# Performance work log

Measured on AMD Instinct MI355X. Metric: run time of the kernel, lower is better.

## Reference

```python
import jax, jax.numpy as jnp
import numpy as np

N = 8192          # batch_size == number of graph nodes
F1 = 64
F2 = 64
D_IN = F1 * F2    # 4096, = int(sqrt(in_feats))**2
D_OUT = 4096      # out_feats, must equal F1*F2 for the final reshape
ALPHA = 0.2       # LeakyReLU negative slope


def setup_inputs() -> dict:
    key = jax.random.key(0)
    k_x, k_w, k_a = jax.random.split(key, 3)
    x = jax.random.normal(k_x, (N, F1, F2), dtype=jnp.float32)
    # torch Linear weight layout: [out_feats, in_feats]; xavier-uniform-ish scale
    lim_w = float(np.sqrt(6.0 / (D_IN + D_OUT)) * np.sqrt(2.0))
    W = jax.random.uniform(k_w, (D_OUT, D_IN), dtype=jnp.float32, minval=-lim_w, maxval=lim_w)
    lim_a = float(np.sqrt(6.0 / (1 + 2 * D_OUT)))
    a = jax.random.uniform(k_a, (1, 2 * D_OUT), dtype=jnp.float32, minval=-lim_a, maxval=lim_a)
    return {"x": x, "W": W, "a": a}


def reference(x, W, a):
    b, f1, f2 = x.shape
    x_flat = x.reshape(b, f1 * f2)                 # [N, D_in]
    h = x_flat @ W.T                               # [N, D_out]
    # scores[i,j] = leakyrelu(cat(h_i, h_j) @ a.T) = leakyrelu(h_i.a1 + h_j.a2)
    a1 = a[0, :D_OUT]                              # [D_out]
    a2 = a[0, D_OUT:]                              # [D_out]
    s1 = h @ a1                                    # [N]
    s2 = h @ a2                                    # [N]
    e = s1[:, None] + s2[None, :]                  # [N, N]
    e = jnp.where(e > 0, e, ALPHA * e)             # LeakyReLU
    attention = jax.nn.softmax(e, axis=-1)         # [N, N]
    # dropout=0.0 (eval-mode / deterministic reference)
    out = attention @ h                            # [N, D_out]
    return out.reshape(b, f1, f2)
```

## Files before the change

kernel.cpp:

```cpp
#include <hip/hip_runtime.h>
#include <hip/hip_bf16.h>
#include <stdint.h>


typedef float  f32x4  __attribute__((ext_vector_type(4)));
typedef __bf16 bf16x8 __attribute__((ext_vector_type(8)));

#define AS1 __attribute__((address_space(1)))
#define AS3 __attribute__((address_space(3)))

constexpr int NB  = 8192;
constexpr int DF  = 4096;
constexpr int CH  = 64;
constexpr int NCH = NB / CH;

constexpr int GK  = DF;
constexpr int BKK = 64;
constexpr int NT2 = GK / BKK;

__device__ __forceinline__ uint16_t f2bf_u(float f) {
  union { float f; uint32_t u; } x; x.f = f;
  return (uint16_t)((x.u + 0x7FFFu + ((x.u >> 16) & 1u)) >> 16);
}
__device__ __forceinline__ float bfu2f(uint16_t v) {
  union { uint32_t u; float f; } x; x.u = ((uint32_t)v) << 16;
  return x.f;
}

__global__ __launch_bounds__(256) void cvt_f32_to_bf16(
    const float* __restrict__ in, uint16_t* __restrict__ out, int n4) {
  int idx = blockIdx.x * 256 + threadIdx.x;
  int stride = gridDim.x * 256;
  for (int i = idx; i < n4; i += stride) {
    float4 v = ((const float4*)in)[i];
    ushort4 o;
    o.x = f2bf_u(v.x); o.y = f2bf_u(v.y); o.z = f2bf_u(v.z); o.w = f2bf_u(v.w);
    ((ushort4*)out)[i] = o;
  }
}


#define STAGE_A(tt, half) do {                                                 \
  const uint16_t* g0_ = Ag + (size_t)((half) * 128) * GK + (size_t)(tt) * BKK; \
  uint32_t d_ = ((uint32_t)((tt) & 1)) * 32768u + (uint32_t)(half) * 8192u +   \
                (uint32_t)wave * 512u;                                         \
  __builtin_amdgcn_global_load_lds((const AS1 void*)g0_,                       \
      (AS3 void*)(lds + d_), 16, 0, 0);                                        \
  __builtin_amdgcn_global_load_lds((const AS1 void*)(g0_ + (size_t)64 * GK),   \
      (AS3 void*)(lds + d_ + 4096u), 16, 0, 0);                                \
} while (0)

#define STAGE_B(tt, half) do {                                                 \
  const uint16_t* g0_ = Bg + (size_t)((half) * 128) * GK + (size_t)(tt) * BKK; \
  uint32_t d_ = ((uint32_t)((tt) & 1)) * 32768u + 16384u +                     \
                (uint32_t)(half) * 8192u + (uint32_t)wave * 512u;              \
  __builtin_amdgcn_global_load_lds((const AS1 void*)g0_,                       \
      (AS3 void*)(lds + d_), 16, 0, 0);                                        \
  __builtin_amdgcn_global_load_lds((const AS1 void*)(g0_ + (size_t)64 * GK),   \
      (AS3 void*)(lds + d_ + 4096u), 16, 0, 0);                                \
} while (0)

#define LDA(mh) do {                                                           \
  _Pragma("unroll") for (int mf = 0; mf < 4; ++mf)                             \
    _Pragma("unroll") for (int ks = 0; ks < 2; ++ks)                           \
      aF[mf][ks] = *(const bf16x8*)(lds + bufo +                               \
          (uint32_t)(wm * 128 + (mh) * 64 + mf * 16 + lr) * 64u +              \
          (uint32_t)((ks * 32 + lg * 8) ^ swl));                               \
} while (0)

#define LDB(nh) do {                                                           \
  _Pragma("unroll") for (int nf = 0; nf < 2; ++nf)                             \
    _Pragma("unroll") for (int ks = 0; ks < 2; ++ks)                           \
      bF[nf][ks] = *(const bf16x8*)(lds + bufo + 16384u +                      \
          (uint32_t)(wn * 64 + (nh) * 32 + nf * 16 + lr) * 64u +               \
          (uint32_t)((ks * 32 + lg * 8) ^ swl));                               \
} while (0)

#define MMA(mh, nh) do {                                                       \
  _Pragma("unroll") for (int ks = 0; ks < 2; ++ks)                             \
    _Pragma("unroll") for (int mf = 0; mf < 4; ++mf)                           \
      _Pragma("unroll") for (int nf = 0; nf < 2; ++nf)                         \
        acc[(mh) * 4 + mf][(nh) * 2 + nf] =                                    \
            __builtin_amdgcn_mfma_f32_16x16x32_bf16(aF[mf][ks], bF[nf][ks],    \
                acc[(mh) * 4 + mf][(nh) * 2 + nf], 0, 0, 0);                   \
} while (0)

__global__ __launch_bounds__(512, 2) void gemm_nt_async(
    const uint16_t* __restrict__ A, const uint16_t* __restrict__ B,
    uint16_t* __restrict__ C) {
  __shared__ uint16_t lds[65536];

  const int tid  = threadIdx.x;
  const int wave = tid >> 6;
  const int lane = tid & 63;
  const int lr   = lane & 15;
  const int lg   = lane >> 4;
  const int wm   = wave >> 2;
  const int wn   = wave & 3;
  const int swl  = (lr & 7) << 3;

  const int bid = blockIdx.x;
  const int swz = (bid & 7) * 64 + (bid >> 3);
  const int bx  = swz & 15;
  const int by  = swz >> 4;
  const int rowBase = by * 256;
  const int colBase = bx * 256;

  const int sr  = tid >> 3;
  const int sch = (tid & 7) ^ (sr & 7);
  const uint16_t* Ag = A + (size_t)(rowBase + sr) * GK + sch * 8;
  const uint16_t* Bg = B + (size_t)(colBase + sr) * GK + sch * 8;

  f32x4 acc[8][4];
#pragma unroll
  for (int mf = 0; mf < 8; ++mf)
#pragma unroll
    for (int nf = 0; nf < 4; ++nf) acc[mf][nf] = (f32x4){0.f, 0.f, 0.f, 0.f};

  STAGE_A(0, 0);
  STAGE_A(0, 1);
  STAGE_B(0, 0);
  STAGE_B(0, 1);
  asm volatile("s_waitcnt vmcnt(0)" ::: "memory");
  __builtin_amdgcn_s_barrier();

  bf16x8 aF[4][2], bF[2][2];

  for (int t = 0; t < NT2; ++t) {
    const uint32_t bufo = ((uint32_t)(t & 1)) * 32768u;

    if (t + 1 < NT2) {
      STAGE_A(t + 1, 0);
      STAGE_A(t + 1, 1);
      STAGE_B(t + 1, 0);
      STAGE_B(t + 1, 1);
    }

    LDA(0); LDB(0);
    MMA(0, 0);
    LDB(1);
    MMA(0, 1);
    LDA(1);
    MMA(1, 1);
    LDB(0);
    MMA(1, 0);

    if (t + 1 < NT2) {
      asm volatile("s_waitcnt vmcnt(0)" ::: "memory");
      __builtin_amdgcn_s_barrier();
    }
  }

  const int r0 = rowBase + wm * 128 + lg * 4;
  const int c0 = colBase + wn * 64 + lr;
#pragma unroll
  for (int mf = 0; mf < 8; ++mf)
#pragma unroll
    for (int nf = 0; nf < 4; ++nf)
#pragma unroll
      for (int e = 0; e < 4; ++e)
        C[(size_t)(r0 + mf * 16 + e) * (size_t)DF + (c0 + nf * 16)] =
            f2bf_u(acc[mf][nf][e]);
}

__global__ __launch_bounds__(256) void s12_kernel(
    const uint16_t* __restrict__ h, const float* __restrict__ a,
    float* __restrict__ s1, float* __restrict__ s2) {
  const int wave = threadIdx.x >> 6, lane = threadIdx.x & 63;
  const int row = blockIdx.x * 4 + wave;
  const uint32_t* hr = (const uint32_t*)(h + (size_t)row * DF);
  float d1 = 0.f, d2 = 0.f;
#pragma unroll 4
  for (int it = 0; it < DF / 128; it++) {
    int u = it * 64 + lane;
    uint32_t hv = hr[u];
    float lo = bfu2f((uint16_t)hv), hi = bfu2f((uint16_t)(hv >> 16));
    int k = 2 * u;
    d1 += a[k] * lo + a[k + 1] * hi;
    d2 += a[DF + k] * lo + a[DF + k + 1] * hi;
  }
  for (int off = 32; off > 0; off >>= 1) {
    d1 += __shfl_down(d1, off, 64);
    d2 += __shfl_down(d2, off, 64);
  }
  if (lane == 0) { s1[row] = d1; s2[row] = d2; }
}

__global__ __launch_bounds__(256) void rank_kernel(
    const float* __restrict__ s2, int* __restrict__ pi,
    float* __restrict__ s2sorted) {
  __shared__ float ld[NB];
  for (int idx = threadIdx.x; idx < NB; idx += 256) ld[idx] = s2[idx];
  __syncthreads();
  const int j = blockIdx.x * 256 + threadIdx.x;
  const float v = ld[j];
  int cnt = 0;
  for (int q = 0; q < NB / 4; q++) {
    float4 u = ((const float4*)ld)[q];
    int jj = q * 4;
    cnt += (u.x > v) || (u.x == v && (jj + 0) < j);
    cnt += (u.y > v) || (u.y == v && (jj + 1) < j);
    cnt += (u.z > v) || (u.z == v && (jj + 2) < j);
    cnt += (u.w > v) || (u.w == v && (jj + 3) < j);
  }
  pi[cnt] = j;
  s2sorted[cnt] = v;
}

__global__ __launch_bounds__(256) void count_kernel(
    const float* __restrict__ s1, const float* __restrict__ s2,
    int* __restrict__ ci) {
  __shared__ float ld[NB];
  for (int idx = threadIdx.x; idx < NB; idx += 256) ld[idx] = s2[idx];
  __syncthreads();
  const int i = blockIdx.x * 256 + threadIdx.x;
  const float thr = -s1[i];
  int cnt = 0;
  for (int q = 0; q < NB / 4; q++) {
    float4 u = ((const float4*)ld)[q];
    cnt += (u.x > thr) + (u.y > thr) + (u.z > thr) + (u.w > thr);
  }
  ci[i] = cnt;
}

__global__ __launch_bounds__(256) void scan_kernel(
    const float* __restrict__ s2sorted, float* __restrict__ Sb,
    float* __restrict__ Sc, float* __restrict__ wbg, float* __restrict__ wcg) {
  __shared__ float pb[256], pc[256];
  const int t = threadIdx.x;
  float sb = 0.f, sc = 0.f;
  for (int c = t * 32; c < t * 32 + 32; c++) {
    float s = s2sorted[c];
    float wb = __expf(0.2f * s), wc = __expf(s);
    wbg[c] = wb; wcg[c] = wc;
    sb += wb; sc += wc;
  }
  pb[t] = sb; pc[t] = sc;
  __syncthreads();
  if (t == 0) {
    float rb = 0.f, rc = 0.f;
    for (int q = 0; q < 256; q++) {
      float tb = pb[q], tc = pc[q];
      pb[q] = rb; pc[q] = rc;
      rb += tb; rc += tc;
    }
    Sb[0] = 0.f; Sc[0] = 0.f;
    Sb[NB] = rb; Sc[NB] = rc;
  }
  __syncthreads();
  float rb = pb[t], rc = pc[t];
  for (int c = t * 32; c < t * 32 + 32; c++) {
    rb += wbg[c]; rc += wcg[c];
    if (c + 1 < NB) { Sb[c + 1] = rb; Sc[c + 1] = rc; }
  }
}

__global__ __launch_bounds__(256) void zero_hist(int* __restrict__ hist) {
  int t = blockIdx.x * 256 + threadIdx.x;
  if (t <= NB) hist[t] = 0;
}

__global__ __launch_bounds__(256) void finalize_kernel(
    const float* __restrict__ s1, const int* __restrict__ ci,
    const float* __restrict__ Sb, const float* __restrict__ Sc,
    float* __restrict__ f1, float* __restrict__ f2, int* __restrict__ hist) {
  const int i = blockIdx.x * 256 + threadIdx.x;
  const float s1i = s1[i];
  const int c = ci[i];
  const float q1 = __expf(0.2f * s1i), q2 = __expf(s1i);
  const float l = q1 * (Sb[NB] - Sb[c]) + q2 * Sc[c];
  f1[i] = q1 / l;
  f2[i] = q2 / l;
  atomicAdd(&hist[c], 1);
}

__global__ __launch_bounds__(256) void bucket_scan(
    const int* __restrict__ hist, int* __restrict__ istart,
    int* __restrict__ cursor) {
  __shared__ int ps[256];
  const int t = threadIdx.x;
  const int lo = t * 33;
  const int hi = min(lo + 33, NB + 1);
  int s = 0;
  for (int b = lo; b < hi; b++) s += hist[b];
  ps[t] = s;
  __syncthreads();
  if (t == 0) {
    int r = 0;
    for (int q = 0; q < 256; q++) { int v = ps[q]; ps[q] = r; r += v; }
  }
  __syncthreads();
  int r = ps[t];
  for (int b = lo; b < hi; b++) { istart[b] = r; cursor[b] = r; r += hist[b]; }
  if (t == 255) istart[NB + 1] = r;
}

__global__ __launch_bounds__(256) void scatter_kernel(
    const int* __restrict__ ci, int* __restrict__ cursor,
    int* __restrict__ ilist) {
  const int i = blockIdx.x * 256 + threadIdx.x;
  const int b = ci[i];
  const int pos = atomicAdd(&cursor[b], 1);
  ilist[pos] = i;
}

__global__ __launch_bounds__(256) void pass1_kernel(
    const uint16_t* __restrict__ h, const int* __restrict__ pi,
    const float* __restrict__ wbg, const float* __restrict__ wcg,
    float* __restrict__ Bct, float* __restrict__ Cct) {
  __shared__ int   pj[CH];
  __shared__ float wb[CH], wc[CH];
  const int t  = threadIdx.x;
  const int cb = blockIdx.x;
  const int k  = blockIdx.y;
  if (t < CH) {
    int g = k * CH + t;
    pj[t] = pi[g]; wb[t] = wbg[g]; wc[t] = wcg[g];
  }
  __syncthreads();
  const int n0 = cb * 1024 + t * 4;
  float b0 = 0.f, b1 = 0.f, b2 = 0.f, b3 = 0.f;
  float c0 = 0.f, c1 = 0.f, c2 = 0.f, c3 = 0.f;
#pragma unroll 8
  for (int c = 0; c < CH; c++) {
    uint2 hv = *(const uint2*)(h + (size_t)pj[c] * DF + n0);
    float h0 = bfu2f((uint16_t)hv.x), h1 = bfu2f((uint16_t)(hv.x >> 16));
    float h2 = bfu2f((uint16_t)hv.y), h3 = bfu2f((uint16_t)(hv.y >> 16));
    float vb = wb[c], vc = wc[c];
    b0 += vb * h0; b1 += vb * h1; b2 += vb * h2; b3 += vb * h3;
    c0 += vc * h0; c1 += vc * h1; c2 += vc * h2; c3 += vc * h3;
  }
  *(float4*)(Bct + (size_t)k * DF + n0) = make_float4(b0, b1, b2, b3);
  *(float4*)(Cct + (size_t)k * DF + n0) = make_float4(c0, c1, c2, c3);
}

__global__ __launch_bounds__(256) void boff_kernel(
    const float* __restrict__ Bct, const float* __restrict__ Cct,
    float* __restrict__ Boff, float* __restrict__ Coff) {
  __shared__ float sB[4][64], sC[4][64];
  const int t   = threadIdx.x;
  const int cl  = t & 63;
  const int seg = t >> 6;
  const int col = blockIdx.x * 64 + cl;
  float sb = 0.f, sc = 0.f;
#pragma unroll 8
  for (int u = 0; u < NCH / 4; u++) {
    int kk = seg * (NCH / 4) + u;
    sb += Bct[(size_t)kk * DF + col];
    sc += Cct[(size_t)kk * DF + col];
  }
  sB[seg][cl] = sb; sC[seg][cl] = sc;
  __syncthreads();
  float rb = 0.f, rc = 0.f;
#pragma unroll
  for (int s = 0; s < 3; s++)
    if (s < seg) { rb += sB[s][cl]; rc += sC[s][cl]; }
#pragma unroll 4
  for (int u = 0; u < NCH / 4; u++) {
    int kk = seg * (NCH / 4) + u;
    Boff[(size_t)kk * DF + col] = rb;
    Coff[(size_t)kk * DF + col] = rc;
    rb += Bct[(size_t)kk * DF + col];
    rc += Cct[(size_t)kk * DF + col];
  }
  if (seg == 3) {
    Boff[(size_t)NCH * DF + col] = rb;
    Coff[(size_t)NCH * DF + col] = rc;
  }
}

__global__ __launch_bounds__(256) void pass2_kernel(
    const uint16_t* __restrict__ h, const int* __restrict__ pi,
    const float* __restrict__ wbg, const float* __restrict__ wcg,
    const float* __restrict__ Boff, const float* __restrict__ Coff,
    const int* __restrict__ istart, const int* __restrict__ ilist,
    const float* __restrict__ f1, const float* __restrict__ f2,
    float* __restrict__ out) {
  __shared__ int   pj[CH];
  __shared__ float wb[CH], wc[CH];
  __shared__ int   se[CH + 2];
  const int t  = threadIdx.x;
  const int cb = blockIdx.x;
  const int k  = blockIdx.y;
  if (t < CH) {
    int g = k * CH + t;
    pj[t] = pi[g]; wb[t] = wbg[g]; wc[t] = wcg[g];
  }
  if (t < CH + 2) se[t] = istart[k * CH + t];
  __syncthreads();
  const int n0 = cb * 1024 + t * 4;
  const float4 An = *(const float4*)(Boff + (size_t)NCH * DF + n0);
  const float4 Bo = *(const float4*)(Boff + (size_t)k * DF + n0);
  const float4 Co = *(const float4*)(Coff + (size_t)k * DF + n0);
  float b0 = Bo.x, b1 = Bo.y, b2 = Bo.z, b3 = Bo.w;
  float c0 = Co.x, c1 = Co.y, c2 = Co.z, c3 = Co.w;

  if (k == 0) {
    for (int idx = se[0]; idx < se[1]; idx++) {
      const int i = ilist[idx];
      const float fa = f1[i];
      *(float4*)(out + (size_t)i * DF + n0) =
          make_float4(fa * An.x, fa * An.y, fa * An.z, fa * An.w);
    }
  }
  for (int c = 0; c < CH; c++) {
    uint2 hv = *(const uint2*)(h + (size_t)pj[c] * DF + n0);
    float h0 = bfu2f((uint16_t)hv.x), h1 = bfu2f((uint16_t)(hv.x >> 16));
    float h2 = bfu2f((uint16_t)hv.y), h3 = bfu2f((uint16_t)(hv.y >> 16));
    float vb = wb[c], vc = wc[c];
    b0 += vb * h0; b1 += vb * h1; b2 += vb * h2; b3 += vb * h3;
    c0 += vc * h0; c1 += vc * h1; c2 += vc * h2; c3 += vc * h3;
    const int e0 = se[c + 1], e1 = se[c + 2];
    for (int idx = e0; idx < e1; idx++) {
      const int i = ilist[idx];
      const float fa = f1[i], fb = f2[i];
      *(float4*)(out + (size_t)i * DF + n0) = make_float4(
          fa * (An.x - b0) + fb * c0, fa * (An.y - b1) + fb * c1,
          fa * (An.z - b2) + fb * c2, fa * (An.w - b3) + fb * c3);
    }
  }
}

extern "C" void kernel_launch(void* const* d_in, const int* in_sizes, int n_in,
                              void* d_out, int out_size, void* d_ws, size_t ws_size,
                              hipStream_t stream) {
  const float* x = (const float*)d_in[0];
  const float* W = (const float*)d_in[1];
  const float* a = (const float*)d_in[2];
  float* out = (float*)d_out;

  char* ws = (char*)d_ws;
  uint16_t* h = (uint16_t*)ws;
  char* sm = ws + 67108864;
  float* s1       = (float*)(sm);
  float* s2       = (float*)(sm + 65536);
  float* s2sorted = (float*)(sm + 131072);
  int*   pi       = (int*)  (sm + 196608);
  int*   ci       = (int*)  (sm + 262144);
  float* Sb       = (float*)(sm + 327680);
  float* Sc       = (float*)(sm + 393216);
  float* wbg      = (float*)(sm + 458752);
  float* wcg      = (float*)(sm + 524288);
  float* f1       = (float*)(sm + 589824);
  float* f2       = (float*)(sm + 655360);
  int*   hist     = (int*)  (sm + 720896);
  int*   istart   = (int*)  (sm + 786432);
  int*   cursor   = (int*)  (sm + 851968);
  int*   ilist    = (int*)  (sm + 917504);
  float* Bct      = (float*)(sm + 1048576);
  float* Cct      = (float*)(sm + 3145728);
  float* Boff     = (float*)(sm + 5242880);
  float* Coff     = (float*)(sm + 7602176);
  char* base2 = ws + 67108864 + 10485760;
  uint16_t* xb = (uint16_t*)base2;
  uint16_t* Wb = (uint16_t*)(base2 + 67108864);

  cvt_f32_to_bf16<<<1024, 256, 0, stream>>>(x, xb, (NB * DF) / 4);
  cvt_f32_to_bf16<<<1024, 256, 0, stream>>>(W, Wb, (DF * DF) / 4);

  gemm_nt_async<<<(NB / 256) * (DF / 256), 512, 0, stream>>>(xb, Wb, h);

  zero_hist<<<33, 256, 0, stream>>>(hist);
  s12_kernel<<<NB / 4, 256, 0, stream>>>(h, a, s1, s2);
  rank_kernel<<<NB / 256, 256, 0, stream>>>(s2, pi, s2sorted);
  count_kernel<<<NB / 256, 256, 0, stream>>>(s1, s2, ci);
  scan_kernel<<<1, 256, 0, stream>>>(s2sorted, Sb, Sc, wbg, wcg);
  finalize_kernel<<<NB / 256, 256, 0, stream>>>(s1, ci, Sb, Sc, f1, f2, hist);
  bucket_scan<<<1, 256, 0, stream>>>(hist, istart, cursor);
  scatter_kernel<<<NB / 256, 256, 0, stream>>>(ci, cursor, ilist);

  pass1_kernel<<<dim3(DF / 1024, NCH), 256, 0, stream>>>(h, pi, wbg, wcg, Bct, Cct);
  boff_kernel<<<DF / 64, 256, 0, stream>>>(Bct, Cct, Boff, Coff);
  pass2_kernel<<<dim3(DF / 1024, NCH), 256, 0, stream>>>(
      h, pi, wbg, wcg, Boff, Coff, istart, ilist, f1, f2, out);
}
```

Baseline: 897.7 us.

## Fuse score dot-products into GEMM epilogue and merge small post-processing kernels

Computes s1/s2 inside the GEMM epilogue from the fp32 accumulators, using wave shuffles and atomic adds, so the separate pass that re-reads h is gone. The s1/s2 buffers are zeroed inside the x conversion kernel. Rank and count become one kernel that splits each row's work across 4 threads. Scan, finalize, histogram and bucket scan move into one single-block kernel with an LDS histogram, and the scatter step moves into pass1. The aim is to cut launch count and an extra read of h. The cost is float atomics with non-deterministic summation order and serial single-block work for the finalize step.

Result: faster. 723.8 us (-19.4%).

```diff
diff --git a/kernel.cpp b/kernel.cpp
--- a/kernel.cpp
+++ b/kernel.cpp
@@ -28,9 +28,13 @@
 }
 
 __global__ __launch_bounds__(256) void cvt_f32_to_bf16(
-    const float* __restrict__ in, uint16_t* __restrict__ out, int n4) {
+    const float* __restrict__ in, uint16_t* __restrict__ out, int n4,
+    float* __restrict__ z1, float* __restrict__ z2, int zn) {
   int idx = blockIdx.x * 256 + threadIdx.x;
   int stride = gridDim.x * 256;
+  if (z1) {
+    for (int g = idx; g < zn; g += stride) { z1[g] = 0.f; z2[g] = 0.f; }
+  }
   for (int i = idx; i < n4; i += stride) {
     float4 v = ((const float4*)in)[i];
     ushort4 o;
@@ -87,7 +91,8 @@
 
 __global__ __launch_bounds__(512, 2) void gemm_nt_async(
     const uint16_t* __restrict__ A, const uint16_t* __restrict__ B,
-    uint16_t* __restrict__ C) {
+    uint16_t* __restrict__ C, const float* __restrict__ a,
+    float* __restrict__ s1g, float* __restrict__ s2g) {
   __shared__ uint16_t lds[65536];
 
   const int tid  = threadIdx.x;
@@ -161,73 +166,81 @@
       for (int e = 0; e < 4; ++e)
         C[(size_t)(r0 + mf * 16 + e) * (size_t)DF + (c0 + nf * 16)] =
             f2bf_u(acc[mf][nf][e]);
-}
-
-__global__ __launch_bounds__(256) void s12_kernel(
-    const uint16_t* __restrict__ h, const float* __restrict__ a,
-    float* __restrict__ s1, float* __restrict__ s2) {
-  const int wave = threadIdx.x >> 6, lane = threadIdx.x & 63;
-  const int row = blockIdx.x * 4 + wave;
-  const uint32_t* hr = (const uint32_t*)(h + (size_t)row * DF);
-  float d1 = 0.f, d2 = 0.f;
-#pragma unroll 4
-  for (int it = 0; it < DF / 128; it++) {
-    int u = it * 64 + lane;
-    uint32_t hv = hr[u];
-    float lo = bfu2f((uint16_t)hv), hi = bfu2f((uint16_t)(hv >> 16));
-    int k = 2 * u;
-    d1 += a[k] * lo + a[k + 1] * hi;
-    d2 += a[DF + k] * lo + a[DF + k + 1] * hi;
-  }
-  for (int off = 32; off > 0; off >>= 1) {
-    d1 += __shfl_down(d1, off, 64);
-    d2 += __shfl_down(d2, off, 64);
-  }
-  if (lane == 0) { s1[row] = d1; s2[row] = d2; }
-}
-
-__global__ __launch_bounds__(256) void rank_kernel(
-    const float* __restrict__ s2, int* __restrict__ pi,
-    float* __restrict__ s2sorted) {
+
+  float a1v[4], a2v[4];
+#pragma unroll
+  for (int nf = 0; nf < 4; ++nf) {
+    int col = c0 + nf * 16;
+    a1v[nf] = a[col];
+    a2v[nf] = a[DF + col];
+  }
+#pragma unroll
+  for (int mf = 0; mf < 8; ++mf) {
+#pragma unroll
+    for (int e = 0; e < 4; ++e) {
+      float p1 = 0.f, p2 = 0.f;
+#pragma unroll
+      for (int nf = 0; nf < 4; ++nf) {
+        float hv = acc[mf][nf][e];
+        p1 += hv * a1v[nf];
+        p2 += hv * a2v[nf];
+      }
+      p1 += __shfl_xor(p1, 1, 64); p1 += __shfl_xor(p1, 2, 64);
+      p1 += __shfl_xor(p1, 4, 64); p1 += __shfl_xor(p1, 8, 64);
+      p2 += __shfl_xor(p2, 1, 64); p2 += __shfl_xor(p2, 2, 64);
+      p2 += __shfl_xor(p2, 4, 64); p2 += __shfl_xor(p2, 8, 64);
+      if (lr == 0) {
+        int row = r0 + mf * 16 + e;
+        atomicAdd(&s1g[row], p1);
+        atomicAdd(&s2g[row], p2);
+      }
+    }
+  }
+}
+
+__global__ __launch_bounds__(256) void rankcount_kernel(
+    const float* __restrict__ s1, const float* __restrict__ s2,
+    int* __restrict__ pi, float* __restrict__ s2sorted, int* __restrict__ ci) {
   __shared__ float ld[NB];
-  for (int idx = threadIdx.x; idx < NB; idx += 256) ld[idx] = s2[idx];
-  __syncthreads();
-  const int j = blockIdx.x * 256 + threadIdx.x;
-  const float v = ld[j];
-  int cnt = 0;
-  for (int q = 0; q < NB / 4; q++) {
+  const int t = threadIdx.x;
+  for (int idx = t; idx < NB; idx += 256) ld[idx] = s2[idx];
+  __syncthreads();
+  const int i    = blockIdx.x * 64 + (t >> 2);
+  const int part = t & 3;
+  const float v   = ld[i];
+  const float thr = -s1[i];
+  int cr = 0, cc = 0;
+  const int q0 = part * (NB / 16);
+  for (int q = q0; q < q0 + NB / 16; q++) {
     float4 u = ((const float4*)ld)[q];
     int jj = q * 4;
-    cnt += (u.x > v) || (u.x == v && (jj + 0) < j);
-    cnt += (u.y > v) || (u.y == v && (jj + 1) < j);
-    cnt += (u.z > v) || (u.z == v && (jj + 2) < j);
-    cnt += (u.w > v) || (u.w == v && (jj + 3) < j);
-  }
-  pi[cnt] = j;
-  s2sorted[cnt] = v;
-}
-
-__global__ __launch_bounds__(256) void count_kernel(
-    const float* __restrict__ s1, const float* __restrict__ s2,
-    int* __restrict__ ci) {
-  __shared__ float ld[NB];
-  for (int idx = threadIdx.x; idx < NB; idx += 256) ld[idx] = s2[idx];
-  __syncthreads();
-  const int i = blockIdx.x * 256 + threadIdx.x;
-  const float thr = -s1[i];
-  int cnt = 0;
-  for (int q = 0; q < NB / 4; q++) {
-    float4 u = ((const float4*)ld)[q];
-    cnt += (u.x > thr) + (u.y > thr) + (u.z > thr) + (u.w > thr);
-  }
-  ci[i] = cnt;
-}
-
-__global__ __launch_bounds__(256) void scan_kernel(
+    cr += (u.x > v) || (u.x == v && (jj + 0) < i);
+    cr += (u.y > v) || (u.y == v && (jj + 1) < i);
+    cr += (u.z > v) || (u.z == v && (jj + 2) < i);
+    cr += (u.w > v) || (u.w == v && (jj + 3) < i);
+    cc += (u.x > thr) + (u.y > thr) + (u.z > thr) + (u.w > thr);
+  }
+  cr += __shfl_xor(cr, 1, 64); cr += __shfl_xor(cr, 2, 64);
+  cc += __shfl_xor(cc, 1, 64); cc += __shfl_xor(cc, 2, 64);
+  if (part == 0) {
+    pi[cr] = i;
+    s2sorted[cr] = v;
+    ci[i] = cc;
+  }
+}
+
+__global__ __launch_bounds__(256) void mega_kernel(
     const float* __restrict__ s2sorted, float* __restrict__ Sb,
-    float* __restrict__ Sc, float* __restrict__ wbg, float* __restrict__ wcg) {
+    float* __restrict__ Sc, float* __restrict__ wbg, float* __restrict__ wcg,
+    const float* __restrict__ s1, const int* __restrict__ ci,
+    float* __restrict__ f1, float* __restrict__ f2,
+    int* __restrict__ istart, int* __restrict__ cursor) {
   __shared__ float pb[256], pc[256];
+  __shared__ int   histL[NB + 1];
+  __shared__ int   ps[256];
   const int t = threadIdx.x;
+  for (int g = t; g <= NB; g += 256) histL[g] = 0;
+
   float sb = 0.f, sc = 0.f;
   for (int c = t * 32; c < t * 32 + 32; c++) {
     float s = s2sorted[c];
@@ -248,71 +261,64 @@
     Sb[NB] = rb; Sc[NB] = rc;
   }
   __syncthreads();
-  float rb = pb[t], rc = pc[t];
-  for (int c = t * 32; c < t * 32 + 32; c++) {
-    rb += wbg[c]; rc += wcg[c];
-    if (c + 1 < NB) { Sb[c + 1] = rb; Sc[c + 1] = rc; }
-  }
-}
-
-__global__ __launch_bounds__(256) void zero_hist(int* __restrict__ hist) {
-  int t = blockIdx.x * 256 + threadIdx.x;
-  if (t <= NB) hist[t] = 0;
-}
-
-__global__ __launch_bounds__(256) void finalize_kernel(
-    const float* __restrict__ s1, const int* __restrict__ ci,
-    const float* __restrict__ Sb, const float* __restrict__ Sc,
-    float* __restrict__ f1, float* __restrict__ f2, int* __restrict__ hist) {
-  const int i = blockIdx.x * 256 + threadIdx.x;
-  const float s1i = s1[i];
-  const int c = ci[i];
-  const float q1 = __expf(0.2f * s1i), q2 = __expf(s1i);
-  const float l = q1 * (Sb[NB] - Sb[c]) + q2 * Sc[c];
-  f1[i] = q1 / l;
-  f2[i] = q2 / l;
-  atomicAdd(&hist[c], 1);
-}
-
-__global__ __launch_bounds__(256) void bucket_scan(
-    const int* __restrict__ hist, int* __restrict__ istart,
-    int* __restrict__ cursor) {
-  __shared__ int ps[256];
-  const int t = threadIdx.x;
-  const int lo = t * 33;
-  const int hi = min(lo + 33, NB + 1);
-  int s = 0;
-  for (int b = lo; b < hi; b++) s += hist[b];
-  ps[t] = s;
-  __syncthreads();
-  if (t == 0) {
-    int r = 0;
-    for (int q = 0; q < 256; q++) { int v = ps[q]; ps[q] = r; r += v; }
-  }
-  __syncthreads();
-  int r = ps[t];
-  for (int b = lo; b < hi; b++) { istart[b] = r; cursor[b] = r; r += hist[b]; }
-  if (t == 255) istart[NB + 1] = r;
-}
-
-__global__ __launch_bounds__(256) void scatter_kernel(
-    const int* __restrict__ ci, int* __restrict__ cursor,
-    int* __restrict__ ilist) {
-  const int i = blockIdx.x * 256 + threadIdx.x;
-  const int b = ci[i];
-  const int pos = atomicAdd(&cursor[b], 1);
-  ilist[pos] = i;
+  {
+    float rb = pb[t], rc = pc[t];
+    for (int c = t * 32; c < t * 32 + 32; c++) {
+      rb += wbg[c]; rc += wcg[c];
+      if (c + 1 < NB) { Sb[c + 1] = rb; Sc[c + 1] = rc; }
+    }
+  }
+  __syncthreads();
+
+  const float SbT = Sb[NB];
+  for (int q = 0; q < NB / 256; q++) {
+    int i = q * 256 + t;
+    float s1i = s1[i];
+    int c = ci[i];
+    float q1 = __expf(0.2f * s1i), q2 = __expf(s1i);
+    float l = q1 * (SbT - Sb[c]) + q2 * Sc[c];
+    f1[i] = q1 / l;
+    f2[i] = q2 / l;
+    atomicAdd(&histL[c], 1);
+  }
+  __syncthreads();
+
+  {
+    const int lo = t * 33;
+    const int hi = min(lo + 33, NB + 1);
+    int s = 0;
+    for (int b = lo; b < hi; b++) s += histL[b];
+    ps[t] = s;
+    __syncthreads();
+    if (t == 0) {
+      int r = 0;
+      for (int q = 0; q < 256; q++) { int v = ps[q]; ps[q] = r; r += v; }
+    }
+    __syncthreads();
+    int r = ps[t];
+    for (int b = lo; b < hi; b++) { istart[b] = r; cursor[b] = r; r += histL[b]; }
+    if (t == 255) istart[NB + 1] = r;
+  }
 }
 
 __global__ __launch_bounds__(256) void pass1_kernel(
     const uint16_t* __restrict__ h, const int* __restrict__ pi,
     const float* __restrict__ wbg, const float* __restrict__ wcg,
-    float* __restrict__ Bct, float* __restrict__ Cct) {
+    float* __restrict__ Bct, float* __restrict__ Cct,
+    const int* __restrict__ ci, int* __restrict__ cursor,
+    int* __restrict__ ilist) {
   __shared__ int   pj[CH];
   __shared__ float wb[CH], wc[CH];
   const int t  = threadIdx.x;
   const int cb = blockIdx.x;
   const int k  = blockIdx.y;
+  const int flat = k * 4 + cb;
+  if (flat < 32) {
+    const int i = flat * 256 + t;
+    const int b = ci[i];
+    const int pos = atomicAdd(&cursor[b], 1);
+    ilist[pos] = i;
+  }
   if (t < CH) {
     int g = k * CH + t;
     pj[t] = pi[g]; wb[t] = wbg[g]; wc[t] = wcg[g];
@@ -443,7 +449,6 @@
   float* wcg      = (float*)(sm + 524288);
   float* f1       = (float*)(sm + 589824);
   float* f2       = (float*)(sm + 655360);
-  int*   hist     = (int*)  (sm + 720896);
   int*   istart   = (int*)  (sm + 786432);
   int*   cursor   = (int*)  (sm + 851968);
   int*   ilist    = (int*)  (sm + 917504);
@@ -455,22 +460,23 @@
   uint16_t* xb = (uint16_t*)base2;
   uint16_t* Wb = (uint16_t*)(base2 + 67108864);
 
-  cvt_f32_to_bf16<<<1024, 256, 0, stream>>>(x, xb, (NB * DF) / 4);
-  cvt_f32_to_bf16<<<1024, 256, 0, stream>>>(W, Wb, (DF * DF) / 4);
-
-  gemm_nt_async<<<(NB / 256) * (DF / 256), 512, 0, stream>>>(xb, Wb, h);
-
-  zero_hist<<<33, 256, 0, stream>>>(hist);
-  s12_kernel<<<NB / 4, 256, 0, stream>>>(h, a, s1, s2);
-  rank_kernel<<<NB / 256, 256, 0, stream>>>(s2, pi, s2sorted);
-  count_kernel<<<NB / 256, 256, 0, stream>>>(s1, s2, ci);
-  scan_kernel<<<1, 256, 0, stream>>>(s2sorted, Sb, Sc, wbg, wcg);
-  finalize_kernel<<<NB / 256, 256, 0, stream>>>(s1, ci, Sb, Sc, f1, f2, hist);
-  bucket_scan<<<1, 256, 0, stream>>>(hist, istart, cursor);
-  scatter_kernel<<<NB / 256, 256, 0, stream>>>(ci, cursor, ilist);
-
-  pass1_kernel<<<dim3(DF / 1024, NCH), 256, 0, stream>>>(h, pi, wbg, wcg, Bct, Cct);
+  cvt_f32_to_bf16<<<1024, 256, 0, stream>>>(x, xb, (NB * DF) / 4, s1, s2, NB);
+  cvt_f32_to_bf16<<<1024, 256, 0, stream>>>(W, Wb, (DF * DF) / 4,
+                                            nullptr, nullptr, 0);
+
+  gemm_nt_async<<<(NB / 256) * (DF / 256), 512, 0, stream>>>(
+      xb, Wb, h, a, s1, s2);
+
+  rankcount_kernel<<<NB / 64, 256, 0, stream>>>(s1, s2, pi, s2sorted, ci);
+
+  mega_kernel<<<1, 256, 0, stream>>>(s2sorted, Sb, Sc, wbg, wcg,
+                                     s1, ci, f1, f2, istart, cursor);
+
+  pass1_kernel<<<dim3(DF / 1024, NCH), 256, 0, stream>>>(
+      h, pi, wbg, wcg, Bct, Cct, ci, cursor, ilist);
+
   boff_kernel<<<DF / 64, 256, 0, stream>>>(Bct, Cct, Boff, Coff);
+
   pass2_kernel<<<dim3(DF / 1024, NCH), 256, 0, stream>>>(
       h, pi, wbg, wcg, Boff, Coff, istart, ilist, f1, f2, out);
 }
```
